# Optimization experiments

Measured on AMD Instinct MI355X. Metric: run time of the kernel, lower is better.

## Reference

```python
import jax, jax.numpy as jnp
import numpy as np

N = 100000
M = 20000
NNZ = 1000000
D_IN = 128
D_OUT = 128


def setup_inputs() -> dict:
    key = jax.random.key(0)
    ks = jax.random.split(key, 6)
    return {
        "node_features": jax.random.normal(ks[0], (N, D_IN), dtype=jnp.float32),
        "data": jax.random.uniform(ks[1], (NNZ,), dtype=jnp.float32),
        "W": jax.random.normal(ks[2], (D_OUT, D_IN), dtype=jnp.float32) / np.sqrt(D_IN),
        "b": jax.random.normal(ks[3], (D_OUT,), dtype=jnp.float32),
        "v_idx": jax.random.randint(ks[4], (NNZ,), 0, N, dtype=jnp.int32),
        "e_idx": jax.random.randint(ks[5], (NNZ,), 0, M, dtype=jnp.int32),
        "n": N,
        "m": M,
    }


def reference(node_features, data, W, b, v_idx, e_idx, n, m):
    # Linear projection (eqx.nn.Linear: y = W @ x + b, vmapped over nodes)
    x = node_features @ W.T + b  # [n, d_out]

    # Degree normalization terms
    d_e = jax.ops.segment_sum(data, e_idx, num_segments=m)  # [m]
    d_v = jax.ops.segment_sum(data, v_idx, num_segments=n)  # [n]
    d_e_inv = jnp.where(d_e > 0, 1.0 / d_e, 0.0)
    d_v_inv = jnp.where(d_v > 0, 1.0 / d_v, 0.0)

    # vertex -> edge: H.T @ x via gather-scale-scatter
    e = jax.ops.segment_sum(x[v_idx] * data[:, None], e_idx, num_segments=m)  # [m, d_out]
    e = e * d_e_inv[:, None]

    # edge -> vertex: H @ e via gather-scale-scatter
    out = jax.ops.segment_sum(e[e_idx] * data[:, None], v_idx, num_segments=n)  # [n, d_out]
    out = out * d_v_inv[:, None]
    return out
```

## Files before the change

kernel.cpp:

```cpp
#include <hip/hip_runtime.h>

#define DF  128
#define PAD 16
#define NB  128
#define ME  20000

typedef float f32x2 __attribute__((ext_vector_type(2)));

__device__ __forceinline__ unsigned bf16rne(float f) {
    unsigned u = __float_as_uint(f);
    return (u + 0x7fffu + ((u >> 16) & 1u)) >> 16;
}

__device__ __forceinline__ unsigned w15enc(float f) {
    unsigned bits = __float_as_uint(f);
    unsigned r = (bits + 0xFFFu + ((bits >> 13) & 1u)) >> 13;
    return (r > (96u << 10)) ? (r - (96u << 10)) : 0u;
}
__device__ __forceinline__ float w15dec(unsigned w) {
    return w ? __uint_as_float((w + (96u << 10)) << 13) : 0.f;
}

#if __has_builtin(__builtin_amdgcn_fdot2_f32_bf16)
typedef __bf16 bf16x2 __attribute__((ext_vector_type(2)));
__device__ __forceinline__ float dot2bf(unsigned a, unsigned b, float c) {
    return __builtin_amdgcn_fdot2_f32_bf16(
        __builtin_bit_cast(bf16x2, a), __builtin_bit_cast(bf16x2, b), c, false);
}
#else
__device__ __forceinline__ float dot2bf(unsigned a, unsigned b, float c) {
    c += __uint_as_float(a << 16) * __uint_as_float(b << 16);
    c += __uint_as_float(a & 0xffff0000u) * __uint_as_float(b & 0xffff0000u);
    return c;
}
#endif

__global__ __launch_bounds__(256) void hist_e_lds(
    const int* __restrict__ vi, const int* __restrict__ ei,
    int* __restrict__ cntV, int* __restrict__ rank,
    int* __restrict__ bhE, int nnz, int epb)
{
    __shared__ int lh[ME];
    for (int k = threadIdx.x; k < ME; k += 256) lh[k] = 0;
    __syncthreads();

    int b = blockIdx.x;
    int lo = b * epb;
    int hi = min(nnz, lo + epb);
    int iters = (epb >> 2) >> 8;
    for (int it = 0; it < iters; ++it) {
        int i = lo + (it * 256 + threadIdx.x) * 4;
        if (i + 4 <= hi) {
            int4 e4 = *(const int4*)(ei + i);
            int4 v4 = *(const int4*)(vi + i);
            int le0 = atomicAdd(&lh[e4.x], 1);
            int le1 = atomicAdd(&lh[e4.y], 1);
            int le2 = atomicAdd(&lh[e4.z], 1);
            int le3 = atomicAdd(&lh[e4.w], 1);
            int rv0 = atomicAdd(&cntV[v4.x * PAD], 1);
            int rv1 = atomicAdd(&cntV[v4.y * PAD], 1);
            int rv2 = atomicAdd(&cntV[v4.z * PAD], 1);
            int rv3 = atomicAdd(&cntV[v4.w * PAD], 1);
            int4 r4 = {le0 | (rv0 << 16), le1 | (rv1 << 16),
                       le2 | (rv2 << 16), le3 | (rv3 << 16)};
            *(int4*)(rank + i) = r4;
        } else {
            for (int j = i; j < hi; ++j) {
                int le = atomicAdd(&lh[ei[j]], 1);
                int rv = atomicAdd(&cntV[vi[j] * PAD], 1);
                rank[j] = le | (rv << 16);
            }
        }
    }
    __syncthreads();
    for (int k = threadIdx.x; k < ME; k += 256)
        bhE[(size_t)b * ME + k] = lh[k];
}

__global__ __launch_bounds__(256) void scanE_conv(
    int* __restrict__ bhE, int* __restrict__ totE,
    const float* __restrict__ nf, const float* __restrict__ W,
    unsigned* __restrict__ nfh, unsigned* __restrict__ wp, int n64)
{
    int k = blockIdx.x * 256 + threadIdx.x;
    if (k < ME) {
        int run = 0;
        #pragma unroll 4
        for (int b = 0; b < NB; ++b) {
            int t = bhE[(size_t)b * ME + k];
            bhE[(size_t)b * ME + k] = run;
            run += t;
        }
        totE[k] = run;
    }
    int tid = blockIdx.x * 256 + threadIdx.x;
    int nth = gridDim.x * 256;
    const float2* __restrict__ in2 = (const float2*)nf;
    for (int i = tid; i < n64; i += nth) {
        float2 f = in2[i];
        nfh[i] = bf16rne(f.x) | (bf16rne(f.y) << 16);
    }
    if (tid < DF * 64) {
        int j = tid >> 6, k2 = tid & 63;
        float2 f = ((const float2*)W)[tid];
        wp[k2 * DF + j] = bf16rne(f.x) | (bf16rne(f.y) << 16);
    }
}

__global__ __launch_bounds__(256) void scan_k1(
    const int* __restrict__ totE, const int* __restrict__ cntV,
    int* __restrict__ bsum, int m, int len)
{
    __shared__ int s[256];
    int tid = threadIdx.x;
    int base = blockIdx.x * 2048 + tid * 8;
    int t = 0;
    #pragma unroll
    for (int i = 0; i < 8; ++i) {
        int idx = base + i;
        if (idx < len) t += (idx < m) ? totE[idx] : cntV[(idx - m) * PAD];
    }
    s[tid] = t; __syncthreads();
    for (int d = 128; d > 0; d >>= 1) {
        if (tid < d) s[tid] += s[tid + d];
        __syncthreads();
    }
    if (tid == 0) bsum[blockIdx.x] = s[0];
}

__global__ __launch_bounds__(256) void scan_k2(int* __restrict__ bsum, int nb)
{
    __shared__ int s[256];
    int t = threadIdx.x;
    int v = (t < nb) ? bsum[t] : 0;
    s[t] = v; __syncthreads();
    for (int d = 1; d < 256; d <<= 1) {
        int u = (t >= d) ? s[t - d] : 0;
        __syncthreads();
        s[t] += u;
        __syncthreads();
    }
    if (t < nb) bsum[t] = s[t] - v;
}

__global__ __launch_bounds__(256) void scan_k3(
    const int* __restrict__ totE, const int* __restrict__ cntV,
    const int* __restrict__ bsum, int* __restrict__ seg, int m, int len)
{
    __shared__ int s[256];
    int tid = threadIdx.x;
    int base = blockIdx.x * 2048 + tid * 8;
    int v[8]; int t = 0;
    #pragma unroll
    for (int i = 0; i < 8; ++i) {
        int idx = base + i;
        v[i] = (idx < len) ? ((idx < m) ? totE[idx] : cntV[(idx - m) * PAD]) : 0;
        t += v[i];
    }
    s[tid] = t; __syncthreads();
    for (int d = 1; d < 256; d <<= 1) {
        int u = (tid >= d) ? s[tid - d] : 0;
        __syncthreads();
        s[tid] += u;
        __syncthreads();
    }
    int run = bsum[blockIdx.x] + (s[tid] - t);
    #pragma unroll
    for (int i = 0; i < 8; ++i) {
        int idx = base + i;
        if (idx < len) { seg[idx] = run; run += v[i]; }
    }
}

__global__ __launch_bounds__(256) void place_kernel(
    const int* __restrict__ vi, const int* __restrict__ ei,
    const float* __restrict__ data, const int* __restrict__ rank,
    const int* __restrict__ seg, const int* __restrict__ bhE,
    unsigned* __restrict__ pair, int nnz, int m, int epb)
{
    int base = (blockIdx.x * 256 + threadIdx.x) * 4;
    if (base + 4 <= nnz) {
        int bH = base / epb;
        const int* __restrict__ bb = bhE + (size_t)bH * ME;
        int4 e4 = *(const int4*)(ei + base);
        int4 v4 = *(const int4*)(vi + base);
        int4 r4 = *(const int4*)(rank + base);
        float4 d4 = *(const float4*)(data + base);
        int ee[4] = {e4.x, e4.y, e4.z, e4.w};
        int vv[4] = {v4.x, v4.y, v4.z, v4.w};
        int rr[4] = {r4.x, r4.y, r4.z, r4.w};
        float dd[4] = {d4.x, d4.y, d4.z, d4.w};
        #pragma unroll
        for (int q = 0; q < 4; ++q) {
            unsigned w15 = w15enc(dd[q]) << 17;
            int pe = seg[ee[q]] + bb[ee[q]] + (rr[q] & 0xffff);
            int pv = seg[m + vv[q]] + (rr[q] >> 16);
            __builtin_nontemporal_store(w15 | (unsigned)vv[q], pair + pe);
            __builtin_nontemporal_store(w15 | (unsigned)ee[q], pair + pv);
        }
    } else {
        for (int i = base; i < nnz; ++i) {
            int bH = i / epb;
            int e = ei[i], v = vi[i], r = rank[i];
            unsigned w15 = w15enc(data[i]) << 17;
            int pe = seg[e] + bhE[(size_t)bH * ME + e] + (r & 0xffff);
            int pv = seg[m + v] + (r >> 16);
            __builtin_nontemporal_store(w15 | (unsigned)v, pair + pe);
            __builtin_nontemporal_store(w15 | (unsigned)e, pair + pv);
        }
    }
}

__global__ __launch_bounds__(256) void gather_y_linear(
    const unsigned* __restrict__ nfh, const int* __restrict__ seg,
    const unsigned* __restrict__ pair, const unsigned* __restrict__ wp,
    const float* __restrict__ b, unsigned* __restrict__ e16, int m)
{
    __shared__ unsigned rowbuf[4][64];
    int wv = threadIdx.x >> 6;
    int wid = (blockIdx.x * 256 + threadIdx.x) >> 6;
    int lane = threadIdx.x & 63;
    if (wid >= m) return;
    int start = seg[wid];
    int end   = seg[wid + 1];
    float ax = 0.f, ay = 0.f, ws = 0.f;
    int k = start;
    for (; k + 16 <= end; k += 16) {
        unsigned p[16];
        #pragma unroll
        for (int q = 0; q < 16; ++q) p[q] = __builtin_nontemporal_load(pair + k + q);
        unsigned u[16];
        #pragma unroll
        for (int q = 0; q < 16; ++q) u[q] = nfh[(size_t)(p[q] & 0x1FFFFu) * 64 + lane];
        #pragma unroll
        for (int q = 0; q < 16; ++q) {
            float w = w15dec(p[q] >> 17);
            ax += w * __uint_as_float(u[q] << 16);
            ay += w * __uint_as_float(u[q] & 0xffff0000u);
            ws += w;
        }
    }
    for (; k + 4 <= end; k += 4) {
        unsigned p[4];
        #pragma unroll
        for (int q = 0; q < 4; ++q) p[q] = __builtin_nontemporal_load(pair + k + q);
        unsigned u[4];
        #pragma unroll
        for (int q = 0; q < 4; ++q) u[q] = nfh[(size_t)(p[q] & 0x1FFFFu) * 64 + lane];
        #pragma unroll
        for (int q = 0; q < 4; ++q) {
            float w = w15dec(p[q] >> 17);
            ax += w * __uint_as_float(u[q] << 16);
            ay += w * __uint_as_float(u[q] & 0xffff0000u);
            ws += w;
        }
    }
    for (; k < end; ++k) {
        unsigned p0 = __builtin_nontemporal_load(pair + k);
        float w0 = w15dec(p0 >> 17);
        unsigned ua = nfh[(size_t)(p0 & 0x1FFFFu) * 64 + lane];
        ax += w0 * __uint_as_float(ua << 16);
        ay += w0 * __uint_as_float(ua & 0xffff0000u);
        ws += w0;
    }
    float inv = (ws > 0.f) ? 1.f / ws : 0.f;
    rowbuf[wv][lane] = bf16rne(ax * inv) | (bf16rne(ay * inv) << 16);

    float2 bb = ((const float2*)b)[lane];
    float acc0 = (ws > 0.f) ? bb.x : 0.f;
    float acc1 = (ws > 0.f) ? bb.y : 0.f;
    const unsigned* __restrict__ row = rowbuf[wv];
    #pragma unroll 8
    for (int k2 = 0; k2 < 64; ++k2) {
        unsigned r = row[k2];
        uint2 u = ((const uint2*)(wp + k2 * DF))[lane];
        acc0 = dot2bf(r, u.x, acc0);
        acc1 = dot2bf(r, u.y, acc1);
    }
    e16[(size_t)wid * 64 + lane] = bf16rne(acc0) | (bf16rne(acc1) << 16);
}

__global__ __launch_bounds__(256) void gather_out(
    const unsigned* __restrict__ e16, const int* __restrict__ seg,
    const unsigned* __restrict__ pair,
    float* __restrict__ out, int n, int m, int tot)
{
    int wid = (blockIdx.x * 256 + threadIdx.x) >> 6;
    int lane = threadIdx.x & 63;
    if (wid >= n) return;
    int idx = m + wid;
    int start = seg[idx];
    int end   = (wid == n - 1) ? tot : seg[idx + 1];
    float ax = 0.f, ay = 0.f, ws = 0.f;
    int k = start;
    for (; k + 16 <= end; k += 16) {
        unsigned p[16];
        #pragma unroll
        for (int q = 0; q < 16; ++q) p[q] = __builtin_nontemporal_load(pair + k + q);
        unsigned u[16];
        #pragma unroll
        for (int q = 0; q < 16; ++q) u[q] = e16[(size_t)(p[q] & 0x1FFFFu) * 64 + lane];
        #pragma unroll
        for (int q = 0; q < 16; ++q) {
            float w = w15dec(p[q] >> 17);
            ax += w * __uint_as_float(u[q] << 16);
            ay += w * __uint_as_float(u[q] & 0xffff0000u);
            ws += w;
        }
    }
    for (; k + 4 <= end; k += 4) {
        unsigned p[4];
        #pragma unroll
        for (int q = 0; q < 4; ++q) p[q] = __builtin_nontemporal_load(pair + k + q);
        unsigned u[4];
        #pragma unroll
        for (int q = 0; q < 4; ++q) u[q] = e16[(size_t)(p[q] & 0x1FFFFu) * 64 + lane];
        #pragma unroll
        for (int q = 0; q < 4; ++q) {
            float w = w15dec(p[q] >> 17);
            ax += w * __uint_as_float(u[q] << 16);
            ay += w * __uint_as_float(u[q] & 0xffff0000u);
            ws += w;
        }
    }
    for (; k < end; ++k) {
        unsigned p0 = __builtin_nontemporal_load(pair + k);
        float w0 = w15dec(p0 >> 17);
        unsigned ua = e16[(size_t)(p0 & 0x1FFFFu) * 64 + lane];
        ax += w0 * __uint_as_float(ua << 16);
        ay += w0 * __uint_as_float(ua & 0xffff0000u);
        ws += w0;
    }
    float inv = (ws > 0.f) ? 1.f / ws : 0.f;
    f32x2 o = {ax * inv, ay * inv};
    __builtin_nontemporal_store(o, (f32x2*)out + (size_t)wid * 64 + lane);
}

extern "C" void kernel_launch(void* const* d_in, const int* in_sizes, int n_in,
                              void* d_out, int out_size, void* d_ws, size_t ws_size,
                              hipStream_t stream)
{
    const float* nf   = (const float*)d_in[0];
    const float* data = (const float*)d_in[1];
    const float* W    = (const float*)d_in[2];
    const float* b    = (const float*)d_in[3];
    const int*   vi   = (const int*)d_in[4];
    const int*   ei   = (const int*)d_in[5];

    const int n   = in_sizes[0] / DF;
    const int nnz = in_sizes[1];
    const int m   = ME;

    const int epb = ((nnz + NB - 1) / NB + 1023) & ~1023;

    int*   seg   = (int*)d_ws;
    int*   bsum  = seg + (m + n);
    int*   totE  = bsum + 256;
    int*   rank  = totE + m;
    unsigned* pair = (unsigned*)(rank + nnz);
    unsigned* e16 = pair + 2 * (size_t)nnz;
    unsigned* wp  = e16 + (size_t)m * 64;
    unsigned* nfh = wp + DF * 64;
    int*   cntV  = (int*)(nfh + (size_t)n * 64);
    int*   bhE   = cntV + (size_t)n * PAD;
    float* out   = (float*)d_out;

    hipMemsetAsync(cntV, 0, (size_t)n * PAD * sizeof(int), stream);

    hist_e_lds<<<NB, 256, 0, stream>>>(vi, ei, cntV, rank, bhE, nnz, epb);

    scanE_conv<<<512, 256, 0, stream>>>(bhE, totE, nf, W, nfh, wp, n * 64);

    int len = m + n;
    int nb = (len + 2047) / 2048;
    scan_k1<<<nb, 256, 0, stream>>>(totE, cntV, bsum, m, len);
    scan_k2<<<1, 256, 0, stream>>>(bsum, nb);
    scan_k3<<<nb, 256, 0, stream>>>(totE, cntV, bsum, seg, m, len);

    int nbQ = (nnz / 4 + 255) / 256;
    place_kernel<<<nbQ, 256, 0, stream>>>(vi, ei, data, rank, seg, bhE,
                                          pair, nnz, m, epb);

    gather_y_linear<<<(m + 3) / 4, 256, 0, stream>>>(nfh, seg, pair, wp, b, e16, m);
    gather_out<<<(n + 3) / 4, 256, 0, stream>>>(e16, seg, pair, out, n, m, 2 * nnz);
}
```

Before: 274.6 us.

## Replace global vertex-count atomics with packed 16-bit LDS histograms and atomic placement

The edge histogram now packs two 16-bit counters per LDS word, so it takes half the shared memory. The vertex histogram, which used padded global atomics plus a memset, is now built in LDS over three vertex partitions, and per-block counts are reduced column-wise. Vertex-side placement no longer stores a rank; it takes positions with an atomicAdd on the segment offsets, so vertex segments become unordered and the gather kernels read shifted boundaries. The aim is to cut global atomic traffic, the large padded count array and its memset, at the cost of re-reading vi three times and doing global atomics in place_kernel.

```diff
diff --git a/kernel.cpp b/kernel.cpp
--- a/kernel.cpp
+++ b/kernel.cpp
@@ -1,9 +1,11 @@
 #include <hip/hip_runtime.h>
 
 #define DF  128
-#define PAD 16
 #define NB  128
 #define ME  20000
+#define EW  10000
+#define VW  16667
+#define VP  3
 
 typedef float f32x2 __attribute__((ext_vector_type(2)));
 
@@ -35,65 +37,105 @@
 }
 #endif
 
-__global__ __launch_bounds__(256) void hist_e_lds(
+__global__ __launch_bounds__(256) void hist_lds(
     const int* __restrict__ vi, const int* __restrict__ ei,
-    int* __restrict__ cntV, int* __restrict__ rank,
-    int* __restrict__ bhE, int nnz, int epb)
-{
-    __shared__ int lh[ME];
-    for (int k = threadIdx.x; k < ME; k += 256) lh[k] = 0;
-    __syncthreads();
-
+    unsigned short* __restrict__ rank,
+    unsigned* __restrict__ bhE, unsigned* __restrict__ bhV, int nnz, int epb)
+{
+    __shared__ unsigned lh[VW];
     int b = blockIdx.x;
     int lo = b * epb;
     int hi = min(nnz, lo + epb);
-    int iters = (epb >> 2) >> 8;
+    int iters = epb >> 10;
+
+    for (int w = threadIdx.x; w < EW; w += 256) lh[w] = 0;
+    __syncthreads();
     for (int it = 0; it < iters; ++it) {
         int i = lo + (it * 256 + threadIdx.x) * 4;
         if (i + 4 <= hi) {
             int4 e4 = *(const int4*)(ei + i);
-            int4 v4 = *(const int4*)(vi + i);
-            int le0 = atomicAdd(&lh[e4.x], 1);
-            int le1 = atomicAdd(&lh[e4.y], 1);
-            int le2 = atomicAdd(&lh[e4.z], 1);
-            int le3 = atomicAdd(&lh[e4.w], 1);
-            int rv0 = atomicAdd(&cntV[v4.x * PAD], 1);
-            int rv1 = atomicAdd(&cntV[v4.y * PAD], 1);
-            int rv2 = atomicAdd(&cntV[v4.z * PAD], 1);
-            int rv3 = atomicAdd(&cntV[v4.w * PAD], 1);
-            int4 r4 = {le0 | (rv0 << 16), le1 | (rv1 << 16),
-                       le2 | (rv2 << 16), le3 | (rv3 << 16)};
-            *(int4*)(rank + i) = r4;
+            int ee[4] = {e4.x, e4.y, e4.z, e4.w};
+            unsigned short r[4];
+            #pragma unroll
+            for (int q = 0; q < 4; ++q) {
+                int sh = (ee[q] & 1) * 16;
+                unsigned ret = atomicAdd(&lh[ee[q] >> 1], 1u << sh);
+                r[q] = (unsigned short)((ret >> sh) & 0xffffu);
+            }
+            *(ushort4*)(rank + i) = ushort4{r[0], r[1], r[2], r[3]};
         } else {
             for (int j = i; j < hi; ++j) {
-                int le = atomicAdd(&lh[ei[j]], 1);
-                int rv = atomicAdd(&cntV[vi[j] * PAD], 1);
-                rank[j] = le | (rv << 16);
+                int e = ei[j]; int sh = (e & 1) * 16;
+                unsigned ret = atomicAdd(&lh[e >> 1], 1u << sh);
+                rank[j] = (unsigned short)((ret >> sh) & 0xffffu);
             }
         }
     }
     __syncthreads();
-    for (int k = threadIdx.x; k < ME; k += 256)
-        bhE[(size_t)b * ME + k] = lh[k];
-}
-
-__global__ __launch_bounds__(256) void scanE_conv(
-    int* __restrict__ bhE, int* __restrict__ totE,
+    for (int w = threadIdx.x; w < EW; w += 256)
+        bhE[(size_t)b * EW + w] = lh[w];
+
+    for (int p = 0; p < VP; ++p) {
+        int vbase = p * (2 * VW);
+        __syncthreads();
+        for (int w = threadIdx.x; w < VW; w += 256) lh[w] = 0;
+        __syncthreads();
+        for (int it = 0; it < iters; ++it) {
+            int i = lo + (it * 256 + threadIdx.x) * 4;
+            if (i + 4 <= hi) {
+                int4 v4 = *(const int4*)(vi + i);
+                int vv[4] = {v4.x, v4.y, v4.z, v4.w};
+                #pragma unroll
+                for (int q = 0; q < 4; ++q) {
+                    int d = vv[q] - vbase;
+                    if (d >= 0 && d < 2 * VW)
+                        atomicAdd(&lh[d >> 1], 1u << ((d & 1) * 16));
+                }
+            } else {
+                for (int j = i; j < hi; ++j) {
+                    int d = vi[j] - vbase;
+                    if (d >= 0 && d < 2 * VW)
+                        atomicAdd(&lh[d >> 1], 1u << ((d & 1) * 16));
+                }
+            }
+        }
+        __syncthreads();
+        for (int w = threadIdx.x; w < VW; w += 256)
+            bhV[(size_t)b * (VP * VW) + p * VW + w] = lh[w];
+    }
+}
+
+__global__ __launch_bounds__(256) void scan_cols_conv(
+    unsigned* __restrict__ bhE, const unsigned* __restrict__ bhV,
+    int* __restrict__ totE, int* __restrict__ totV,
     const float* __restrict__ nf, const float* __restrict__ W,
-    unsigned* __restrict__ nfh, unsigned* __restrict__ wp, int n64)
-{
-    int k = blockIdx.x * 256 + threadIdx.x;
-    if (k < ME) {
-        int run = 0;
+    unsigned* __restrict__ nfh, unsigned* __restrict__ wp, int n, int n64)
+{
+    int tid = blockIdx.x * 256 + threadIdx.x;
+    if (tid < EW) {
+        unsigned run0 = 0, run1 = 0;
         #pragma unroll 4
         for (int b = 0; b < NB; ++b) {
-            int t = bhE[(size_t)b * ME + k];
-            bhE[(size_t)b * ME + k] = run;
-            run += t;
-        }
-        totE[k] = run;
-    }
-    int tid = blockIdx.x * 256 + threadIdx.x;
+            unsigned w = bhE[(size_t)b * EW + tid];
+            unsigned c0 = w & 0xffffu, c1 = w >> 16;
+            bhE[(size_t)b * EW + tid] = run0 | (run1 << 16);
+            run0 += c0; run1 += c1;
+        }
+        totE[2 * tid] = (int)run0;
+        totE[2 * tid + 1] = (int)run1;
+    } else if (tid < EW + VP * VW) {
+        int w = tid - EW;
+        unsigned s0 = 0, s1 = 0;
+        #pragma unroll 4
+        for (int b = 0; b < NB; ++b) {
+            unsigned x = bhV[(size_t)b * (VP * VW) + w];
+            s0 += x & 0xffffu; s1 += x >> 16;
+        }
+        int p = w / VW, wi = w - p * VW;
+        int k0 = p * (2 * VW) + 2 * wi;
+        if (k0 < n) totV[k0] = (int)s0;
+        if (k0 + 1 < n) totV[k0 + 1] = (int)s1;
+    }
     int nth = gridDim.x * 256;
     const float2* __restrict__ in2 = (const float2*)nf;
     for (int i = tid; i < n64; i += nth) {
@@ -108,7 +150,7 @@
 }
 
 __global__ __launch_bounds__(256) void scan_k1(
-    const int* __restrict__ totE, const int* __restrict__ cntV,
+    const int* __restrict__ totE, const int* __restrict__ totV,
     int* __restrict__ bsum, int m, int len)
 {
     __shared__ int s[256];
@@ -118,7 +160,7 @@
     #pragma unroll
     for (int i = 0; i < 8; ++i) {
         int idx = base + i;
-        if (idx < len) t += (idx < m) ? totE[idx] : cntV[(idx - m) * PAD];
+        if (idx < len) t += (idx < m) ? totE[idx] : totV[idx - m];
     }
     s[tid] = t; __syncthreads();
     for (int d = 128; d > 0; d >>= 1) {
@@ -144,7 +186,7 @@
 }
 
 __global__ __launch_bounds__(256) void scan_k3(
-    const int* __restrict__ totE, const int* __restrict__ cntV,
+    const int* __restrict__ totE, const int* __restrict__ totV,
     const int* __restrict__ bsum, int* __restrict__ seg, int m, int len)
 {
     __shared__ int s[256];
@@ -154,7 +196,7 @@
     #pragma unroll
     for (int i = 0; i < 8; ++i) {
         int idx = base + i;
-        v[i] = (idx < len) ? ((idx < m) ? totE[idx] : cntV[(idx - m) * PAD]) : 0;
+        v[i] = (idx < len) ? ((idx < m) ? totE[idx] : totV[idx - m]) : 0;
         t += v[i];
     }
     s[tid] = t; __syncthreads();
@@ -174,37 +216,40 @@
 
 __global__ __launch_bounds__(256) void place_kernel(
     const int* __restrict__ vi, const int* __restrict__ ei,
-    const float* __restrict__ data, const int* __restrict__ rank,
-    const int* __restrict__ seg, const int* __restrict__ bhE,
+    const float* __restrict__ data, const unsigned short* __restrict__ rank,
+    int* __restrict__ seg, const unsigned* __restrict__ bhE,
     unsigned* __restrict__ pair, int nnz, int m, int epb)
 {
     int base = (blockIdx.x * 256 + threadIdx.x) * 4;
     if (base + 4 <= nnz) {
         int bH = base / epb;
-        const int* __restrict__ bb = bhE + (size_t)bH * ME;
+        const unsigned* __restrict__ bb = bhE + (size_t)bH * EW;
         int4 e4 = *(const int4*)(ei + base);
         int4 v4 = *(const int4*)(vi + base);
-        int4 r4 = *(const int4*)(rank + base);
+        ushort4 r4 = *(const ushort4*)(rank + base);
         float4 d4 = *(const float4*)(data + base);
         int ee[4] = {e4.x, e4.y, e4.z, e4.w};
         int vv[4] = {v4.x, v4.y, v4.z, v4.w};
-        int rr[4] = {r4.x, r4.y, r4.z, r4.w};
+        unsigned short rr[4] = {r4.x, r4.y, r4.z, r4.w};
         float dd[4] = {d4.x, d4.y, d4.z, d4.w};
         #pragma unroll
         for (int q = 0; q < 4; ++q) {
             unsigned w15 = w15enc(dd[q]) << 17;
-            int pe = seg[ee[q]] + bb[ee[q]] + (rr[q] & 0xffff);
-            int pv = seg[m + vv[q]] + (rr[q] >> 16);
+            unsigned bword = bb[ee[q] >> 1];
+            int baseE = (int)((bword >> ((ee[q] & 1) * 16)) & 0xffffu);
+            int pe = seg[ee[q]] + baseE + rr[q];
+            int pv = atomicAdd(&seg[m + vv[q]], 1);
             __builtin_nontemporal_store(w15 | (unsigned)vv[q], pair + pe);
             __builtin_nontemporal_store(w15 | (unsigned)ee[q], pair + pv);
         }
     } else {
         for (int i = base; i < nnz; ++i) {
-            int bH = i / epb;
-            int e = ei[i], v = vi[i], r = rank[i];
+            int e = ei[i], v = vi[i];
             unsigned w15 = w15enc(data[i]) << 17;
-            int pe = seg[e] + bhE[(size_t)bH * ME + e] + (r & 0xffff);
-            int pv = seg[m + v] + (r >> 16);
+            unsigned bword = bhE[(size_t)(i / epb) * EW + (e >> 1)];
+            int baseE = (int)((bword >> ((e & 1) * 16)) & 0xffffu);
+            int pe = seg[e] + baseE + rank[i];
+            int pv = atomicAdd(&seg[m + v], 1);
             __builtin_nontemporal_store(w15 | (unsigned)v, pair + pe);
             __builtin_nontemporal_store(w15 | (unsigned)e, pair + pv);
         }
@@ -214,7 +259,7 @@
 __global__ __launch_bounds__(256) void gather_y_linear(
     const unsigned* __restrict__ nfh, const int* __restrict__ seg,
     const unsigned* __restrict__ pair, const unsigned* __restrict__ wp,
-    const float* __restrict__ b, unsigned* __restrict__ e16, int m)
+    const float* __restrict__ b, unsigned* __restrict__ e16, int m, int nnz)
 {
     __shared__ unsigned rowbuf[4][64];
     int wv = threadIdx.x >> 6;
@@ -222,7 +267,7 @@
     int lane = threadIdx.x & 63;
     if (wid >= m) return;
     int start = seg[wid];
-    int end   = seg[wid + 1];
+    int end   = (wid == m - 1) ? nnz : seg[wid + 1];
     float ax = 0.f, ay = 0.f, ws = 0.f;
     int k = start;
     for (; k + 16 <= end; k += 16) {
@@ -283,14 +328,13 @@
 __global__ __launch_bounds__(256) void gather_out(
     const unsigned* __restrict__ e16, const int* __restrict__ seg,
     const unsigned* __restrict__ pair,
-    float* __restrict__ out, int n, int m, int tot)
+    float* __restrict__ out, int n, int m, int nnz)
 {
     int wid = (blockIdx.x * 256 + threadIdx.x) >> 6;
     int lane = threadIdx.x & 63;
     if (wid >= n) return;
-    int idx = m + wid;
-    int start = seg[idx];
-    int end   = (wid == n - 1) ? tot : seg[idx + 1];
+    int start = wid ? seg[m + wid - 1] : nnz;
+    int end   = seg[m + wid];
     float ax = 0.f, ay = 0.f, ws = 0.f;
     int k = start;
     for (; k + 16 <= end; k += 16) {
@@ -356,31 +400,32 @@
     int*   seg   = (int*)d_ws;
     int*   bsum  = seg + (m + n);
     int*   totE  = bsum + 256;
-    int*   rank  = totE + m;
+    int*   totV  = totE + m;
+    unsigned short* rank = (unsigned short*)(totV + n);
     unsigned* pair = (unsigned*)(rank + nnz);
     unsigned* e16 = pair + 2 * (size_t)nnz;
     unsigned* wp  = e16 + (size_t)m * 64;
     unsigned* nfh = wp + DF * 64;
-    int*   cntV  = (int*)(nfh + (size_t)n * 64);
-    int*   bhE   = cntV + (size_t)n * PAD;
+    unsigned* bhE = nfh + (size_t)n * 64;
+    unsigned* bhV = bhE + (size_t)NB * EW;
     float* out   = (float*)d_out;
 
-    hipMemsetAsync(cntV, 0, (size_t)n * PAD * sizeof(int), stream);
-
-    hist_e_lds<<<NB, 256, 0, stream>>>(vi, ei, cntV, rank, bhE, nnz, epb);
-
-    scanE_conv<<<512, 256, 0, stream>>>(bhE, totE, nf, W, nfh, wp, n * 64);
+    hist_lds<<<NB, 256, 0, stream>>>(vi, ei, rank, bhE, bhV, nnz, epb);
+
+    scan_cols_conv<<<512, 256, 0, stream>>>(bhE, bhV, totE, totV,
+                                            nf, W, nfh, wp, n, n * 64);
 
     int len = m + n;
     int nb = (len + 2047) / 2048;
-    scan_k1<<<nb, 256, 0, stream>>>(totE, cntV, bsum, m, len);
+    scan_k1<<<nb, 256, 0, stream>>>(totE, totV, bsum, m, len);
     scan_k2<<<1, 256, 0, stream>>>(bsum, nb);
-    scan_k3<<<nb, 256, 0, stream>>>(totE, cntV, bsum, seg, m, len);
+    scan_k3<<<nb, 256, 0, stream>>>(totE, totV, bsum, seg, m, len);
 
     int nbQ = (nnz / 4 + 255) / 256;
     place_kernel<<<nbQ, 256, 0, stream>>>(vi, ei, data, rank, seg, bhE,
                                           pair, nnz, m, epb);
 
-    gather_y_linear<<<(m + 3) / 4, 256, 0, stream>>>(nfh, seg, pair, wp, b, e16, m);
-    gather_out<<<(n + 3) / 4, 256, 0, stream>>>(e16, seg, pair, out, n, m, 2 * nnz);
-}
+    gather_y_linear<<<(m + 3) / 4, 256, 0, stream>>>(nfh, seg, pair, wp, b,
+                                                     e16, m, nnz);
+    gather_out<<<(n + 3) / 4, 256, 0, stream>>>(e16, seg, pair, out, n, m, nnz);
+}
```

After: 266.7 us. -2.9%, faster.
